# Optimization experiments

Hardware: AMD Instinct MI355X
Metric: run time of the kernel (lower is better)

The kernel has to match this reference:

```python
import jax, jax.numpy as jnp
import numpy as np

K = 3          # kernel size (3x3 branch of SConv_2d)
STRIDE = 1
PAD = 1
NONCENTER = jnp.array([0, 1, 2, 3, 5, 6, 7, 8])      # drop center (idx 4) before sort
REORDER = jnp.array([0, 1, 2, 3, 8, 4, 5, 6, 7])     # reinsert center in the middle


def setup_inputs() -> dict:
    key = jax.random.key(0)
    k1, k2, k3, k4 = jax.random.split(key, 4)
    B, Cin, H, Wd = 8, 64, 128, 128
    Cout = 128
    x = jax.random.normal(k1, (B, Cin, H, Wd), dtype=jnp.float32)
    Coefficient = jax.random.normal(k2, (K * K, K * K), dtype=jnp.float32)
    W = jax.random.normal(k3, (Cout, Cin, K, K), dtype=jnp.float32) * 0.05
    b = jax.random.normal(k4, (Cout,), dtype=jnp.float32) * 0.05
    return {"x": x, "Coefficient": Coefficient, "W": W, "b": b}


def reference(x, Coefficient, W, b):
    # pad (same=False -> constant padding PAD on all sides)
    xp = jnp.pad(x, ((0, 0), (0, 0), (PAD, PAD), (PAD, PAD)))
    B, C, Hp, Wp = xp.shape
    Ho = (Hp - K) // STRIDE + 1
    Wo = (Wp - K) // STRIDE + 1
    # unfold: patches[b, kh*K+kw, c, h, w] == torch unfold+view+permute layout [B, KH*KW, C, H*W]
    patches = jnp.stack(
        [xp[:, :, i:i + Ho * STRIDE:STRIDE, j:j + Wo * STRIDE:STRIDE]
         for i in range(K) for j in range(K)], axis=1)           # [B, 9, C, Ho, Wo]
    center = patches[:, 4:5]                                      # [B, 1, C, Ho, Wo]
    y = jnp.einsum('bjchw,ij->bichw', patches, Coefficient)       # [B, 9, C, Ho, Wo]
    ys = jnp.sort(y[:, NONCENTER], axis=1)                        # sort 8 non-center taps
    z = jnp.concatenate([ys, center], axis=1)                     # [B, 9, C, Ho, Wo]
    z = z[:, REORDER]
    # view(B, KH, KW, C, H, W).permute(0,3,4,1,5,2) -> [B, C, KH*H, KW*W]
    z = z.reshape(B, K, K, C, Ho, Wo).transpose(0, 3, 4, 1, 5, 2).reshape(B, C, K * Ho, K * Wo)
    out = jax.lax.conv_general_dilated(
        z, W, window_strides=(K, K), padding='VALID',
        dimension_numbers=('NCHW', 'OIHW', 'NCHW'))
    return out + b[None, :, None, None]
```

## Files before the change

### kernel.cpp

```cpp
#include <hip/hip_runtime.h>
#include <hip/hip_bf16.h>


#define B_   8
#define C_   64
#define H_   128
#define W_   128
#define CO_  128
#define K_   576
#define MT   32
#define SROW 584

typedef __attribute__((ext_vector_type(8))) short  short8;
typedef __attribute__((ext_vector_type(8))) __bf16 bf16x8;
typedef __attribute__((ext_vector_type(4))) float  f32x4;
typedef __attribute__((ext_vector_type(2))) float  f32x2;

__device__ __forceinline__ void cswap2(f32x2 &a, f32x2 &b) {
    f32x2 lo = __builtin_elementwise_min(a, b);
    f32x2 hi = __builtin_elementwise_max(a, b);
    a = lo; b = hi;
}

__device__ __forceinline__ ushort f2bf(float f) {
    union { float f; unsigned u; } v; v.f = f;
    unsigned r = v.u + 0x7fffu + ((v.u >> 16) & 1u);
    return (ushort)(r >> 16);
}

__device__ __forceinline__ unsigned pack2bf(float lo, float hi) {
    union { __hip_bfloat162 h; unsigned u; } cv;
    cv.h = __float22bfloat162_rn(make_float2(lo, hi));
    return cv.u;
}

__global__ __launch_bounds__(256) void conv_W_bf16(const float* __restrict__ Wg,
                                                   ushort* __restrict__ Wb) {
    int i = blockIdx.x * 256 + threadIdx.x;
    if (i < CO_ * K_) Wb[i] = f2bf(Wg[i]);
}

__global__ __launch_bounds__(512, 8) void sconv_mfma(
    const float* __restrict__ x,
    const float* __restrict__ Coef,
    const ushort* __restrict__ Wb,
    const float* __restrict__ bias,
    float* __restrict__ out)
{
    __shared__ __align__(16) ushort Zl[MT * SROW];

    const int tid = threadIdx.x;
    const int bx  = blockIdx.x;
    const int wq  = bx & 7;
    const int hp  = (bx >> 3) & 63;
    const int b   = bx >> 9;
    const int w0  = wq * 16;
    const int h0  = hp * 2;

    {
        const int c  = tid >> 3;
        const int pw = tid & 7;
        const int w  = w0 + pw * 2;
        const float* xb = x + ((size_t)(b * C_ + c)) * (H_ * W_);

        float r[4][4];
        const bool interior = (h0 >= 2) && (h0 <= 124) && (w0 >= 16) && (w0 <= 96);
        if (interior) {
            const float* bp = xb + (h0 - 1) * W_ + (w - 1);
            #pragma unroll
            for (int dy = 0; dy < 4; ++dy) {
                float4 v; __builtin_memcpy(&v, bp + dy * W_, 16);
                r[dy][0] = v.x; r[dy][1] = v.y; r[dy][2] = v.z; r[dy][3] = v.w;
            }
        } else {
            const int wm = w - 1;
            const int wc = min(max(wm, 0), W_ - 4);
            const int s  = wm - wc;
            #pragma unroll
            for (int dy = 0; dy < 4; ++dy) {
                const int hy  = h0 + dy - 1;
                const bool hok = (unsigned)hy < (unsigned)H_;
                const int hc  = min(max(hy, 0), H_ - 1);
                float4 v; __builtin_memcpy(&v, xb + hc * W_ + wc, 16);
                const float rr0 = (s < 0) ? 0.f : ((s > 0) ? v.y : v.x);
                const float rr1 = (s < 0) ? v.x : ((s > 0) ? v.z : v.y);
                const float rr2 = (s < 0) ? v.y : ((s > 0) ? v.w : v.z);
                const float rr3 = (s < 0) ? v.z : ((s > 0) ? 0.f : v.w);
                r[dy][0] = hok ? rr0 : 0.f;
                r[dy][1] = hok ? rr1 : 0.f;
                r[dy][2] = hok ? rr2 : 0.f;
                r[dy][3] = hok ? rr3 : 0.f;
            }
        }

        const int k0 = c * 9;
        #pragma unroll
        for (int hl = 0; hl < 2; ++hl) {
            f32x2 p2[9];
            #pragma unroll
            for (int dy = 0; dy < 3; ++dy)
                #pragma unroll
                for (int dx = 0; dx < 3; ++dx)
                    p2[dy * 3 + dx] = (f32x2){ r[hl + dy][dx], r[hl + dy][dx + 1] };

            f32x2 v2[8];
            #pragma unroll
            for (int ii = 0; ii < 8; ++ii) {
                const int i = ii + (ii >> 2);
                f32x2 acc = p2[0] * Coef[i * 9];
                #pragma unroll
                for (int j = 1; j < 9; ++j) acc += p2[j] * Coef[i * 9 + j];
                v2[ii] = acc;
            }

            cswap2(v2[0],v2[1]); cswap2(v2[2],v2[3]); cswap2(v2[4],v2[5]); cswap2(v2[6],v2[7]);
            cswap2(v2[0],v2[2]); cswap2(v2[1],v2[3]); cswap2(v2[4],v2[6]); cswap2(v2[5],v2[7]);
            cswap2(v2[1],v2[2]); cswap2(v2[5],v2[6]);
            cswap2(v2[0],v2[4]); cswap2(v2[1],v2[5]); cswap2(v2[2],v2[6]); cswap2(v2[3],v2[7]);
            cswap2(v2[2],v2[4]); cswap2(v2[3],v2[5]);
            cswap2(v2[1],v2[2]); cswap2(v2[3],v2[4]); cswap2(v2[5],v2[6]);

            f32x2 z2[9] = { v2[0], v2[1], v2[2], v2[3], p2[4],
                            v2[4], v2[5], v2[6], v2[7] };

            ushort* zr0 = &Zl[(hl * 16 + pw * 2    ) * SROW];
            ushort* zr1 = &Zl[(hl * 16 + pw * 2 + 1) * SROW];
            if ((k0 & 1) == 0) {
                #pragma unroll
                for (int q = 0; q < 4; ++q) {
                    *(unsigned*)&zr0[k0 + 2*q] = pack2bf(z2[2*q][0], z2[2*q+1][0]);
                    *(unsigned*)&zr1[k0 + 2*q] = pack2bf(z2[2*q][1], z2[2*q+1][1]);
                }
                zr0[k0 + 8] = f2bf(z2[8][0]);
                zr1[k0 + 8] = f2bf(z2[8][1]);
            } else {
                zr0[k0] = f2bf(z2[0][0]);
                zr1[k0] = f2bf(z2[0][1]);
                #pragma unroll
                for (int q = 0; q < 4; ++q) {
                    *(unsigned*)&zr0[k0 + 1 + 2*q] = pack2bf(z2[1+2*q][0], z2[2+2*q][0]);
                    *(unsigned*)&zr1[k0 + 1 + 2*q] = pack2bf(z2[1+2*q][1], z2[2+2*q][1]);
                }
            }
        }
    }
    __syncthreads();

    const int wave = tid >> 6;
    const int lane = tid & 63;
    const int quad = lane >> 4;
    const int l16  = lane & 15;

    const ushort* arow0 = &Zl[l16 * SROW];
    const ushort* arow1 = &Zl[(l16 + 16) * SROW];
    const ushort* brow  = Wb + (size_t)(wave * 16 + l16) * K_ + quad * 8;

    f32x4 acc0 = {0.f,0.f,0.f,0.f}, acc1 = acc0;

    #pragma unroll
    for (int ks = 0; ks < 18; ++ks) {
        const int ko = ks * 32 + quad * 8;
        bf16x8 a0 = *(const bf16x8*)(arow0 + ko);
        bf16x8 a1 = *(const bf16x8*)(arow1 + ko);
        bf16x8 bb = __builtin_bit_cast(bf16x8, *(const short8*)(brow + ks * 32));
        acc0 = __builtin_amdgcn_mfma_f32_16x16x32_bf16(a0, bb, acc0, 0, 0, 0);
        acc1 = __builtin_amdgcn_mfma_f32_16x16x32_bf16(a1, bb, acc1, 0, 0, 0);
    }

    const int co = wave * 16 + l16;
    const float bv = bias[co];
    float* o0 = out + (((size_t)(b * CO_ + co)) * H_ + h0) * W_ + w0 + quad * 4;
    float* o1 = o0 + W_;
    *(float4*)o0 = make_float4(acc0.x + bv, acc0.y + bv, acc0.z + bv, acc0.w + bv);
    *(float4*)o1 = make_float4(acc1.x + bv, acc1.y + bv, acc1.z + bv, acc1.w + bv);
}

#define WT 16
__device__ __forceinline__ void cswap(float &a, float &b) {
    float lo = fminf(a, b);
    float hi = fmaxf(a, b);
    a = lo; b = hi;
}
__global__ __launch_bounds__(256) void sconv_fp32(
    const float* __restrict__ x, const float* __restrict__ Coef,
    const float* __restrict__ Wg, const float* __restrict__ bias,
    float* __restrict__ out)
{
    __shared__ float Cf[81];
    __shared__ float Zl[C_ * 9 * WT];
    const int tid = threadIdx.x;
    const int bx  = blockIdx.x;
    const int wt  = bx & 7;
    const int h   = (bx >> 3) & 127;
    const int b   = bx >> 10;
    const int w0  = wt * WT;
    if (tid < 81) Cf[tid] = Coef[tid];
    __syncthreads();
    for (int task = tid; task < C_ * WT; task += 256) {
        const int c = task >> 4, wl = task & 15, w = w0 + wl;
        const float* xb = x + (b * C_ + c) * H_ * W_;
        float p[9];
        #pragma unroll
        for (int dy = 0; dy < 3; ++dy) {
            const int hy = h + dy - 1; const bool hin = (unsigned)hy < (unsigned)H_;
            #pragma unroll
            for (int dx = 0; dx < 3; ++dx) {
                const int wx = w + dx - 1; const bool win = (unsigned)wx < (unsigned)W_;
                p[dy * 3 + dx] = (hin && win) ? xb[hy * W_ + wx] : 0.0f;
            }
        }
        float v[8];
        #pragma unroll
        for (int ii = 0; ii < 8; ++ii) {
            const int i = ii + (ii >> 2);
            float acc = 0.0f;
            #pragma unroll
            for (int j = 0; j < 9; ++j) acc = fmaf(Cf[i * 9 + j], p[j], acc);
            v[ii] = acc;
        }
        cswap(v[0], v[1]); cswap(v[2], v[3]); cswap(v[4], v[5]); cswap(v[6], v[7]);
        cswap(v[0], v[2]); cswap(v[1], v[3]); cswap(v[4], v[6]); cswap(v[5], v[7]);
        cswap(v[1], v[2]); cswap(v[5], v[6]);
        cswap(v[0], v[4]); cswap(v[1], v[5]); cswap(v[2], v[6]); cswap(v[3], v[7]);
        cswap(v[2], v[4]); cswap(v[3], v[5]);
        cswap(v[1], v[2]); cswap(v[3], v[4]); cswap(v[5], v[6]);
        const int base = c * 9 * WT + wl;
        Zl[base + 0*WT]=v[0]; Zl[base + 1*WT]=v[1]; Zl[base + 2*WT]=v[2]; Zl[base + 3*WT]=v[3];
        Zl[base + 4*WT]=p[4];
        Zl[base + 5*WT]=v[4]; Zl[base + 6*WT]=v[5]; Zl[base + 7*WT]=v[6]; Zl[base + 8*WT]=v[7];
    }
    __syncthreads();
    const int co = tid >> 1, w0l = (tid & 1) * 8;
    float acc[8];
    #pragma unroll
    for (int i = 0; i < 8; ++i) acc[i] = 0.0f;
    for (int c = 0; c < C_; ++c) {
        #pragma unroll
        for (int t = 0; t < 9; ++t) {
            const float wv = Wg[(co * C_ + c) * 9 + t];
            const float* zp = &Zl[(c * 9 + t) * WT + w0l];
            const float4 za = *(const float4*)zp;
            const float4 zb = *(const float4*)(zp + 4);
            acc[0]=fmaf(za.x,wv,acc[0]); acc[1]=fmaf(za.y,wv,acc[1]);
            acc[2]=fmaf(za.z,wv,acc[2]); acc[3]=fmaf(za.w,wv,acc[3]);
            acc[4]=fmaf(zb.x,wv,acc[4]); acc[5]=fmaf(zb.y,wv,acc[5]);
            acc[6]=fmaf(zb.z,wv,acc[6]); acc[7]=fmaf(zb.w,wv,acc[7]);
        }
    }
    const float bv = bias[co];
    float* op = out + ((b * CO_ + co) * H_ + h) * W_ + w0 + w0l;
    *(float4*)(op)     = make_float4(acc[0]+bv, acc[1]+bv, acc[2]+bv, acc[3]+bv);
    *(float4*)(op + 4) = make_float4(acc[4]+bv, acc[5]+bv, acc[6]+bv, acc[7]+bv);
}

extern "C" void kernel_launch(void* const* d_in, const int* in_sizes, int n_in,
                              void* d_out, int out_size, void* d_ws, size_t ws_size,
                              hipStream_t stream) {
    const float* x    = (const float*)d_in[0];
    const float* Coef = (const float*)d_in[1];
    const float* Wg   = (const float*)d_in[2];
    const float* bias = (const float*)d_in[3];
    float* out = (float*)d_out;

    const size_t need = (size_t)CO_ * K_ * sizeof(ushort);
    if (ws_size >= need) {
        ushort* Wb = (ushort*)d_ws;
        conv_W_bf16<<<(CO_ * K_ + 255) / 256, 256, 0, stream>>>(Wg, Wb);
        sconv_mfma<<<B_ * (H_ / 2) * (W_ / 16), 512, 0, stream>>>(x, Coef, Wb, bias, out);
    } else {
        sconv_fp32<<<B_ * H_ * 8, 256, 0, stream>>>(x, Coef, Wg, bias, out);
    }
}
```

Baseline: 162.2 us.

## Enlarge tile to 64 pixels, use 32x32x16 MFMA, swizzle LDS, pre-pack weights

Each block now covers 4 output rows instead of 2 (64 pixels), and its 8 waves form a 2x4 grid of 32x32 MFMA tiles using mfma_f32_32x32x16_bf16. The weight conversion kernel writes weights already laid out in the per-lane MFMA fragment order, so each B load is one contiguous coalesced access. Z tiles in LDS use an XOR swizzle and a wider row stride to cut bank conflicts. Bigger tiles halve the number of blocks and reuse each x halo row more, but LDS use doubles and occupancy drops (launch bounds go from 8 to 4).

After: 139.1 us. 1.17x faster.

```diff
diff --git a/kernel.cpp b/kernel.cpp
--- a/kernel.cpp
+++ b/kernel.cpp
@@ -8,13 +8,13 @@
 #define W_   128
 #define CO_  128
 #define K_   576
-#define MT   32
-#define SROW 584
-
-typedef __attribute__((ext_vector_type(8))) short  short8;
-typedef __attribute__((ext_vector_type(8))) __bf16 bf16x8;
-typedef __attribute__((ext_vector_type(4))) float  f32x4;
-typedef __attribute__((ext_vector_type(2))) float  f32x2;
+#define MT   64
+#define SROW 600
+
+typedef __attribute__((ext_vector_type(8)))  short  short8;
+typedef __attribute__((ext_vector_type(8)))  __bf16 bf16x8;
+typedef __attribute__((ext_vector_type(16))) float  f32x16;
+typedef __attribute__((ext_vector_type(2)))  float  f32x2;
 
 __device__ __forceinline__ void cswap2(f32x2 &a, f32x2 &b) {
     f32x2 lo = __builtin_elementwise_min(a, b);
@@ -37,10 +37,18 @@
 __global__ __launch_bounds__(256) void conv_W_bf16(const float* __restrict__ Wg,
                                                    ushort* __restrict__ Wb) {
     int i = blockIdx.x * 256 + threadIdx.x;
-    if (i < CO_ * K_) Wb[i] = f2bf(Wg[i]);
-}
-
-__global__ __launch_bounds__(512, 8) void sconv_mfma(
+    if (i >= CO_ * K_) return;
+    const int e    = i & 7;
+    const int lane = (i >> 3) & 63;
+    const int t    = i >> 9;
+    const int nt   = t / 36;
+    const int ks   = t - nt * 36;
+    const int co   = nt * 32 + (lane & 31);
+    const int k    = ks * 16 + (lane >> 5) * 8 + e;
+    Wb[i] = f2bf(Wg[co * K_ + k]);
+}
+
+__global__ __launch_bounds__(512, 4) void sconv_mfma(
     const float* __restrict__ x,
     const float* __restrict__ Coef,
     const ushort* __restrict__ Wb,
@@ -52,10 +60,10 @@
     const int tid = threadIdx.x;
     const int bx  = blockIdx.x;
     const int wq  = bx & 7;
-    const int hp  = (bx >> 3) & 63;
-    const int b   = bx >> 9;
+    const int hq  = (bx >> 3) & 31;
+    const int b   = bx >> 8;
     const int w0  = wq * 16;
-    const int h0  = hp * 2;
+    const int h0  = hq * 4;
 
     {
         const int c  = tid >> 3;
@@ -63,12 +71,12 @@
         const int w  = w0 + pw * 2;
         const float* xb = x + ((size_t)(b * C_ + c)) * (H_ * W_);
 
-        float r[4][4];
-        const bool interior = (h0 >= 2) && (h0 <= 124) && (w0 >= 16) && (w0 <= 96);
+        float r[6][4];
+        const bool interior = (h0 >= 4) && (h0 <= 120) && (w0 >= 16) && (w0 <= 96);
         if (interior) {
             const float* bp = xb + (h0 - 1) * W_ + (w - 1);
             #pragma unroll
-            for (int dy = 0; dy < 4; ++dy) {
+            for (int dy = 0; dy < 6; ++dy) {
                 float4 v; __builtin_memcpy(&v, bp + dy * W_, 16);
                 r[dy][0] = v.x; r[dy][1] = v.y; r[dy][2] = v.z; r[dy][3] = v.w;
             }
@@ -77,7 +85,7 @@
             const int wc = min(max(wm, 0), W_ - 4);
             const int s  = wm - wc;
             #pragma unroll
-            for (int dy = 0; dy < 4; ++dy) {
+            for (int dy = 0; dy < 6; ++dy) {
                 const int hy  = h0 + dy - 1;
                 const bool hok = (unsigned)hy < (unsigned)H_;
                 const int hc  = min(max(hy, 0), H_ - 1);
@@ -94,8 +102,9 @@
         }
 
         const int k0 = c * 9;
-        #pragma unroll
-        for (int hl = 0; hl < 2; ++hl) {
+        const int sw = pw << 4;
+        #pragma unroll
+        for (int hl = 0; hl < 4; ++hl) {
             f32x2 p2[9];
             #pragma unroll
             for (int dy = 0; dy < 3; ++dy)
@@ -123,23 +132,23 @@
             f32x2 z2[9] = { v2[0], v2[1], v2[2], v2[3], p2[4],
                             v2[4], v2[5], v2[6], v2[7] };
 
-            ushort* zr0 = &Zl[(hl * 16 + pw * 2    ) * SROW];
-            ushort* zr1 = &Zl[(hl * 16 + pw * 2 + 1) * SROW];
+            char* zb0 = (char*)Zl + (size_t)(hl * 16 + pw * 2) * (SROW * 2);
+            char* zb1 = zb0 + SROW * 2;
             if ((k0 & 1) == 0) {
                 #pragma unroll
                 for (int q = 0; q < 4; ++q) {
-                    *(unsigned*)&zr0[k0 + 2*q] = pack2bf(z2[2*q][0], z2[2*q+1][0]);
-                    *(unsigned*)&zr1[k0 + 2*q] = pack2bf(z2[2*q][1], z2[2*q+1][1]);
+                    *(unsigned*)(zb0 + (((k0 + 2*q) * 2) ^ sw)) = pack2bf(z2[2*q][0], z2[2*q+1][0]);
+                    *(unsigned*)(zb1 + (((k0 + 2*q) * 2) ^ sw)) = pack2bf(z2[2*q][1], z2[2*q+1][1]);
                 }
-                zr0[k0 + 8] = f2bf(z2[8][0]);
-                zr1[k0 + 8] = f2bf(z2[8][1]);
+                *(ushort*)(zb0 + (((k0 + 8) * 2) ^ sw)) = f2bf(z2[8][0]);
+                *(ushort*)(zb1 + (((k0 + 8) * 2) ^ sw)) = f2bf(z2[8][1]);
             } else {
-                zr0[k0] = f2bf(z2[0][0]);
-                zr1[k0] = f2bf(z2[0][1]);
+                *(ushort*)(zb0 + ((k0 * 2) ^ sw)) = f2bf(z2[0][0]);
+                *(ushort*)(zb1 + ((k0 * 2) ^ sw)) = f2bf(z2[0][1]);
                 #pragma unroll
                 for (int q = 0; q < 4; ++q) {
-                    *(unsigned*)&zr0[k0 + 1 + 2*q] = pack2bf(z2[1+2*q][0], z2[2+2*q][0]);
-                    *(unsigned*)&zr1[k0 + 1 + 2*q] = pack2bf(z2[1+2*q][1], z2[2+2*q][1]);
+                    *(unsigned*)(zb0 + (((k0 + 1 + 2*q) * 2) ^ sw)) = pack2bf(z2[1+2*q][0], z2[2+2*q][0]);
+                    *(unsigned*)(zb1 + (((k0 + 1 + 2*q) * 2) ^ sw)) = pack2bf(z2[1+2*q][1], z2[2+2*q][1]);
                 }
             }
         }
@@ -148,31 +157,37 @@
 
     const int wave = tid >> 6;
     const int lane = tid & 63;
-    const int quad = lane >> 4;
-    const int l16  = lane & 15;
-
-    const ushort* arow0 = &Zl[l16 * SROW];
-    const ushort* arow1 = &Zl[(l16 + 16) * SROW];
-    const ushort* brow  = Wb + (size_t)(wave * 16 + l16) * K_ + quad * 8;
-
-    f32x4 acc0 = {0.f,0.f,0.f,0.f}, acc1 = acc0;
+    const int mt   = wave >> 2;
+    const int nt   = wave & 3;
+    const int r31  = lane & 31;
+    const int u    = lane >> 5;
+
+    const int arow = mt * 32 + r31;
+    const char* abase = (const char*)Zl + (size_t)arow * (SROW * 2);
+    const int aswz = ((arow >> 1) & 7) << 4;
+    const ushort* bptr = Wb + ((size_t)(nt * 36) * 64 + lane) * 8;
+
+    f32x16 acc = {};
 
     #pragma unroll
-    for (int ks = 0; ks < 18; ++ks) {
-        const int ko = ks * 32 + quad * 8;
-        bf16x8 a0 = *(const bf16x8*)(arow0 + ko);
-        bf16x8 a1 = *(const bf16x8*)(arow1 + ko);
-        bf16x8 bb = __builtin_bit_cast(bf16x8, *(const short8*)(brow + ks * 32));
-        acc0 = __builtin_amdgcn_mfma_f32_16x16x32_bf16(a0, bb, acc0, 0, 0, 0);
-        acc1 = __builtin_amdgcn_mfma_f32_16x16x32_bf16(a1, bb, acc1, 0, 0, 0);
-    }
-
-    const int co = wave * 16 + l16;
+    for (int ks = 0; ks < 36; ++ks) {
+        bf16x8 a  = *(const bf16x8*)(abase + ((ks * 32 + u * 16) ^ aswz));
+        bf16x8 bb = __builtin_bit_cast(bf16x8, *(const short8*)(bptr + ks * 512));
+        acc = __builtin_amdgcn_mfma_f32_32x32x16_bf16(a, bb, acc, 0, 0, 0);
+    }
+
+    const int co = nt * 32 + r31;
     const float bv = bias[co];
-    float* o0 = out + (((size_t)(b * CO_ + co)) * H_ + h0) * W_ + w0 + quad * 4;
-    float* o1 = o0 + W_;
-    *(float4*)o0 = make_float4(acc0.x + bv, acc0.y + bv, acc0.z + bv, acc0.w + bv);
-    *(float4*)o1 = make_float4(acc1.x + bv, acc1.y + bv, acc1.z + bv, acc1.w + bv);
+    float* obase = out + (((size_t)(b * CO_ + co)) * H_ + h0 + mt * 2) * W_ + w0;
+    #pragma unroll
+    for (int qq = 0; qq < 4; ++qq) {
+        const int roff = qq * 8 + u * 4;
+        const int hl   = roff >> 4;
+        const int wl   = roff & 15;
+        float4 vv = make_float4(acc[qq*4+0] + bv, acc[qq*4+1] + bv,
+                                acc[qq*4+2] + bv, acc[qq*4+3] + bv);
+        *(float4*)(obase + hl * W_ + wl) = vv;
+    }
 }
 
 #define WT 16
@@ -266,7 +281,7 @@
     if (ws_size >= need) {
         ushort* Wb = (ushort*)d_ws;
         conv_W_bf16<<<(CO_ * K_ + 255) / 256, 256, 0, stream>>>(Wg, Wb);
-        sconv_mfma<<<B_ * (H_ / 2) * (W_ / 16), 512, 0, stream>>>(x, Coef, Wb, bias, out);
+        sconv_mfma<<<B_ * (H_ / 4) * (W_ / 16), 512, 0, stream>>>(x, Coef, Wb, bias, out);
     } else {
         sconv_fp32<<<B_ * H_ * 8, 256, 0, stream>>>(x, Coef, Wg, bias, out);
     }
```
